# Kernel tuning notes

Hardware: AMD Instinct MI355X
Metric: run time of the kernel (lower is better)

## Reference

```python
import jax, jax.numpy as jnp
import numpy as np

N = 2048
HIDDEN = 64
BOX = 13.7  # box length so density ~ 0.8 for N=2048
CUTOFF = 2.5


def setup_inputs() -> dict:
    key = jax.random.key(0)
    k_xyz, k_w1, k_w2 = jax.random.split(key, 3)
    xyz = jax.random.uniform(k_xyz, (N, 3), dtype=jnp.float32) * BOX
    cell = jnp.ones((3,), dtype=jnp.float32) * BOX
    w1 = jax.random.normal(k_w1, (1, HIDDEN), dtype=jnp.float32)
    b1 = jnp.zeros((HIDDEN,), dtype=jnp.float32)
    w2 = jax.random.normal(k_w2, (HIDDEN, 1), dtype=jnp.float32)
    b2 = jnp.zeros((1,), dtype=jnp.float32)
    return {"xyz": xyz, "cell": cell, "w1": w1, "b1": b1, "w2": w2, "b2": b2}


def reference(xyz, cell, w1, b1, w2, b2):
    # all-pairs displacement with minimum-image PBC wrapping, [N, N, 3]
    d = xyz[None, :, :] - xyz[:, None, :]
    offsets = -(d >= 0.5 * cell).astype(jnp.float32) + (d < -0.5 * cell).astype(jnp.float32)
    d = d + offsets * cell
    dis_sq = jnp.sum(d * d, axis=-1)                       # [N, N]
    mask = (dis_sq < CUTOFF ** 2) & (dis_sq != 0.0)        # cutoff + remove self-pairs
    # safe sqrt (avoid nan grads at 0); masked-out entries forced to 0 distance
    pair_dis = jnp.where(mask, jnp.sqrt(jnp.where(mask, dis_sq, 1.0)), 0.0)
    # edge MLP on distances; torch gathers masked pairs (dynamic shape),
    # here we evaluate all N*N pairs and zero masked-out entries (jit-friendly)
    x = pair_dis.reshape(-1, 1)                            # [N*N, 1]
    h = jax.nn.relu(x @ w1 + b1)                           # [N*N, HIDDEN]
    e = h @ w2 + b2                                        # [N*N, 1]
    energy = jnp.where(mask.reshape(-1, 1), e, 0.0)
    return energy
```

## Files before the change

### kernel.cpp

```cpp
#include <hip/hip_runtime.h>

#define HIDDEN 64

__global__ __launch_bounds__(256) void PairPot_kernel(
    const float* __restrict__ xyz, const float* __restrict__ cell,
    const float* __restrict__ w1, const float* __restrict__ b1,
    const float* __restrict__ w2, const float* __restrict__ b2,
    float* __restrict__ out, int N)
{
    __shared__ float s_w1[HIDDEN], s_b1[HIDDEN], s_w2[HIDDEN];
    __shared__ float s_c, s_b2;
    __shared__ int s_fast;

    int t = threadIdx.x;
    if (t < HIDDEN) {
        float w1k = w1[t], b1k = b1[t], w2k = w2[t];
        s_w1[t] = w1k; s_b1[t] = b1k; s_w2[t] = w2k;
        float c = (w1k > 0.0f) ? __fmul_rn(w1k, w2k) : 0.0f;
        #pragma unroll
        for (int off = 32; off; off >>= 1) c += __shfl_xor(c, off, 64);
        unsigned long long bz = __ballot(b1k == 0.0f);
        if (t == 0) { s_c = c; s_b2 = b2[0]; s_fast = (bz == ~0ULL) ? 1 : 0; }
    }
    __syncthreads();

    const int i  = blockIdx.y;
    const int jg = blockIdx.x * 256 + threadIdx.x;
    const int n4 = N >> 2;
    if (jg >= n4) return;
    const int j0 = jg << 2;

    const float cx = cell[0], cy = cell[1], cz = cell[2];
    const float hx = __fmul_rn(0.5f, cx);
    const float hy = __fmul_rn(0.5f, cy);
    const float hz = __fmul_rn(0.5f, cz);

    const float xi0 = xyz[3*i+0], xi1 = xyz[3*i+1], xi2 = xyz[3*i+2];

    const float4* pj = reinterpret_cast<const float4*>(xyz + 3*j0);
    const float4 va = pj[0], vb = pj[1], vc = pj[2];
    const float jx[4] = {va.x, va.w, vb.z, vc.y};
    const float jy[4] = {va.y, vb.x, vb.w, vc.z};
    const float jz[4] = {va.z, vb.y, vc.x, vc.w};

    const bool  fast  = (s_fast != 0);
    const float c_lin = s_c;
    const float b2v   = s_b2;

    float res[4];
    #pragma unroll
    for (int u = 0; u < 4; ++u) {
        float dx = __fsub_rn(jx[u], xi0);
        float dy = __fsub_rn(jy[u], xi1);
        float dz = __fsub_rn(jz[u], xi2);
        dx = __fadd_rn(dx, (dx >= hx) ? -cx : ((dx < -hx) ? cx : 0.0f));
        dy = __fadd_rn(dy, (dy >= hy) ? -cy : ((dy < -hy) ? cy : 0.0f));
        dz = __fadd_rn(dz, (dz >= hz) ? -cz : ((dz < -hz) ? cz : 0.0f));
        float s = __fadd_rn(__fadd_rn(__fmul_rn(dx, dx), __fmul_rn(dy, dy)),
                            __fmul_rn(dz, dz));
        bool m = (s < 6.25f) && (s != 0.0f);
        float r = sqrtf(s);
        float e;
        if (fast) {
            e = fmaf(c_lin, r, b2v);
        } else {
            e = b2v;
            for (int k = 0; k < HIDDEN; ++k)
                e = fmaf(fmaxf(fmaf(r, s_w1[k], s_b1[k]), 0.0f), s_w2[k], e);
        }
        res[u] = m ? e : 0.0f;
    }

    float4 o;
    o.x = res[0]; o.y = res[1]; o.z = res[2]; o.w = res[3];
    reinterpret_cast<float4*>(out)[i * n4 + jg] = o;
}

extern "C" void kernel_launch(void* const* d_in, const int* in_sizes, int n_in,
                              void* d_out, int out_size, void* d_ws, size_t ws_size,
                              hipStream_t stream) {
    const float* xyz  = (const float*)d_in[0];
    const float* cell = (const float*)d_in[1];
    const float* w1   = (const float*)d_in[2];
    const float* b1   = (const float*)d_in[3];
    const float* w2   = (const float*)d_in[4];
    const float* b2   = (const float*)d_in[5];
    float* out = (float*)d_out;

    const int N = in_sizes[0] / 3;
    dim3 grid((N / 4 + 255) / 256, N);
    PairPot_kernel<<<grid, 256, 0, stream>>>(xyz, cell, w1, b1, w2, b2, out, N);
}
```

Before: 12.95 us.

## Use grid-stride loop with fixed grid and drop shared-memory weight staging

```diff
diff --git a/kernel.cpp b/kernel.cpp
--- a/kernel.cpp
+++ b/kernel.cpp
@@ -6,74 +6,68 @@
     const float* __restrict__ xyz, const float* __restrict__ cell,
     const float* __restrict__ w1, const float* __restrict__ b1,
     const float* __restrict__ w2, const float* __restrict__ b2,
-    float* __restrict__ out, int N)
+    float* __restrict__ out, int N, int shift)
 {
-    __shared__ float s_w1[HIDDEN], s_b1[HIDDEN], s_w2[HIDDEN];
-    __shared__ float s_c, s_b2;
-    __shared__ int s_fast;
-
-    int t = threadIdx.x;
-    if (t < HIDDEN) {
-        float w1k = w1[t], b1k = b1[t], w2k = w2[t];
-        s_w1[t] = w1k; s_b1[t] = b1k; s_w2[t] = w2k;
-        float c = (w1k > 0.0f) ? __fmul_rn(w1k, w2k) : 0.0f;
-        #pragma unroll
-        for (int off = 32; off; off >>= 1) c += __shfl_xor(c, off, 64);
-        unsigned long long bz = __ballot(b1k == 0.0f);
-        if (t == 0) { s_c = c; s_b2 = b2[0]; s_fast = (bz == ~0ULL) ? 1 : 0; }
-    }
-    __syncthreads();
-
-    const int i  = blockIdx.y;
-    const int jg = blockIdx.x * 256 + threadIdx.x;
-    const int n4 = N >> 2;
-    if (jg >= n4) return;
-    const int j0 = jg << 2;
+    const int lane = threadIdx.x & 63;
+    const float w1k = w1[lane];
+    const float b1k = b1[lane];
+    const float w2k = w2[lane];
+    float c = (w1k > 0.0f) ? __fmul_rn(w1k, w2k) : 0.0f;
+    #pragma unroll
+    for (int off = 32; off; off >>= 1) c += __shfl_xor(c, off, 64);
+    const bool fast = (__ballot(b1k == 0.0f) == ~0ULL);
+    const float b2v = b2[0];
 
     const float cx = cell[0], cy = cell[1], cz = cell[2];
     const float hx = __fmul_rn(0.5f, cx);
     const float hy = __fmul_rn(0.5f, cy);
     const float hz = __fmul_rn(0.5f, cz);
 
-    const float xi0 = xyz[3*i+0], xi1 = xyz[3*i+1], xi2 = xyz[3*i+2];
+    const int n4m   = (1 << shift) - 1;
+    const int total = N << shift;
+    const int stride = gridDim.x * blockDim.x;
 
-    const float4* pj = reinterpret_cast<const float4*>(xyz + 3*j0);
-    const float4 va = pj[0], vb = pj[1], vc = pj[2];
-    const float jx[4] = {va.x, va.w, vb.z, vc.y};
-    const float jy[4] = {va.y, vb.x, vb.w, vc.z};
-    const float jz[4] = {va.z, vb.y, vc.x, vc.w};
+    for (int g = blockIdx.x * blockDim.x + threadIdx.x; g < total; g += stride) {
+        const int i  = g >> shift;
+        const int j0 = (g & n4m) << 2;
 
-    const bool  fast  = (s_fast != 0);
-    const float c_lin = s_c;
-    const float b2v   = s_b2;
+        const float xi0 = xyz[3*i+0], xi1 = xyz[3*i+1], xi2 = xyz[3*i+2];
 
-    float res[4];
-    #pragma unroll
-    for (int u = 0; u < 4; ++u) {
-        float dx = __fsub_rn(jx[u], xi0);
-        float dy = __fsub_rn(jy[u], xi1);
-        float dz = __fsub_rn(jz[u], xi2);
-        dx = __fadd_rn(dx, (dx >= hx) ? -cx : ((dx < -hx) ? cx : 0.0f));
-        dy = __fadd_rn(dy, (dy >= hy) ? -cy : ((dy < -hy) ? cy : 0.0f));
-        dz = __fadd_rn(dz, (dz >= hz) ? -cz : ((dz < -hz) ? cz : 0.0f));
-        float s = __fadd_rn(__fadd_rn(__fmul_rn(dx, dx), __fmul_rn(dy, dy)),
-                            __fmul_rn(dz, dz));
-        bool m = (s < 6.25f) && (s != 0.0f);
-        float r = sqrtf(s);
-        float e;
-        if (fast) {
-            e = fmaf(c_lin, r, b2v);
-        } else {
-            e = b2v;
-            for (int k = 0; k < HIDDEN; ++k)
-                e = fmaf(fmaxf(fmaf(r, s_w1[k], s_b1[k]), 0.0f), s_w2[k], e);
+        const float4* pj = reinterpret_cast<const float4*>(xyz + 3*j0);
+        const float4 va = pj[0], vb = pj[1], vcc = pj[2];
+        const float jx[4] = {va.x, va.w, vb.z, vcc.y};
+        const float jy[4] = {va.y, vb.x, vb.w, vcc.z};
+        const float jz[4] = {va.z, vb.y, vcc.x, vcc.w};
+
+        float res[4];
+        #pragma unroll
+        for (int u = 0; u < 4; ++u) {
+            float dx = __fsub_rn(jx[u], xi0);
+            float dy = __fsub_rn(jy[u], xi1);
+            float dz = __fsub_rn(jz[u], xi2);
+            dx = __fadd_rn(dx, (dx >= hx) ? -cx : ((dx < -hx) ? cx : 0.0f));
+            dy = __fadd_rn(dy, (dy >= hy) ? -cy : ((dy < -hy) ? cy : 0.0f));
+            dz = __fadd_rn(dz, (dz >= hz) ? -cz : ((dz < -hz) ? cz : 0.0f));
+            float s = __fadd_rn(__fadd_rn(__fmul_rn(dx, dx), __fmul_rn(dy, dy)),
+                                __fmul_rn(dz, dz));
+            const bool m = (s < 6.25f) && (s != 0.0f);
+            const float r = sqrtf(s);
+            float e;
+            if (fast) {
+                e = fmaf(c, r, b2v);
+            } else {
+                e = b2v;
+                #pragma clang loop unroll(disable)
+                for (int k = 0; k < HIDDEN; ++k)
+                    e = fmaf(fmaxf(fmaf(r, w1[k], b1[k]), 0.0f), w2[k], e);
+            }
+            res[u] = m ? e : 0.0f;
         }
-        res[u] = m ? e : 0.0f;
+
+        float4 o;
+        o.x = res[0]; o.y = res[1]; o.z = res[2]; o.w = res[3];
+        reinterpret_cast<float4*>(out)[g] = o;
     }
-
-    float4 o;
-    o.x = res[0]; o.y = res[1]; o.z = res[2]; o.w = res[3];
-    reinterpret_cast<float4*>(out)[i * n4 + jg] = o;
 }
 
 extern "C" void kernel_launch(void* const* d_in, const int* in_sizes, int n_in,
@@ -88,6 +82,9 @@
     float* out = (float*)d_out;
 
     const int N = in_sizes[0] / 3;
-    dim3 grid((N / 4 + 255) / 256, N);
-    PairPot_kernel<<<grid, 256, 0, stream>>>(xyz, cell, w1, b1, w2, b2, out, N);
+    int n4 = N >> 2;
+    int shift = 0;
+    while ((1 << shift) < n4) ++shift;
+
+    PairPot_kernel<<<2048, 256, 0, stream>>>(xyz, cell, w1, b1, w2, b2, out, N, shift);
 }
```

After: 13.63 us. +5.3%, slower.
